# Optimization experiments

Measured on AMD Instinct MI355X. Metric: run time of the kernel, lower is better.

The kernel has to match this reference:

```python
import jax, jax.numpy as jnp
import numpy as np


def _gru_layer(x, W_ih, W_hh, b_ih, b_hh):
    # x: [B, T, in]; W_ih: [3H, in]; W_hh: [3H, H]; gate order (r, z, n) as in PyTorch.
    B, T, _ = x.shape
    H = W_hh.shape[1]
    # Precompute input-side gate pre-activations for the whole sequence (batched GEMM).
    gi = jnp.einsum('bti,gi->btg', x, W_ih) + b_ih  # [B, T, 3H]

    def step(h, gi_t):
        gh = h @ W_hh.T + b_hh                      # [B, 3H]
        i_r, i_z, i_n = jnp.split(gi_t, 3, axis=-1)
        h_r, h_z, h_n = jnp.split(gh, 3, axis=-1)
        r = jax.nn.sigmoid(i_r + h_r)
        z = jax.nn.sigmoid(i_z + h_z)
        n = jnp.tanh(i_n + r * h_n)
        h_new = (1.0 - z) * n + z * h
        return h_new, h_new

    h0 = jnp.zeros((B, H), x.dtype)
    _, hs = jax.lax.scan(step, h0, jnp.swapaxes(gi, 0, 1))  # hs: [T, B, H]
    return jnp.swapaxes(hs, 0, 1)                            # [B, T, H]


def setup_inputs() -> dict:
    key = jax.random.key(0)
    ks = jax.random.split(key, 11)
    B, T, I, H, O = 512, 512, 64, 128, 1
    s = 0.1  # keep gate pre-activations out of saturation
    return {
        'x':     jax.random.normal(ks[0], (B, T, I), jnp.float32),
        'W_ih0': jax.random.normal(ks[1], (3 * H, I), jnp.float32) * s,
        'W_hh0': jax.random.normal(ks[2], (3 * H, H), jnp.float32) * s,
        'b_ih0': jax.random.normal(ks[3], (3 * H,), jnp.float32) * s,
        'b_hh0': jax.random.normal(ks[4], (3 * H,), jnp.float32) * s,
        'W_ih1': jax.random.normal(ks[5], (3 * H, H), jnp.float32) * s,
        'W_hh1': jax.random.normal(ks[6], (3 * H, H), jnp.float32) * s,
        'b_ih1': jax.random.normal(ks[7], (3 * H,), jnp.float32) * s,
        'b_hh1': jax.random.normal(ks[8], (3 * H,), jnp.float32) * s,
        'W_fc':  jax.random.normal(ks[9], (O, H), jnp.float32) * s,
        'b_fc':  jax.random.normal(ks[10], (O,), jnp.float32) * s,
    }


def reference(x, W_ih0, W_hh0, b_ih0, b_hh0, W_ih1, W_hh1, b_ih1, b_hh1, W_fc, b_fc):
    h1 = _gru_layer(x, W_ih0, W_hh0, b_ih0, b_hh0)   # [B, T, H]
    h2 = _gru_layer(h1, W_ih1, W_hh1, b_ih1, b_hh1)  # [B, T, H]
    return h2[:, -1, :] @ W_fc.T + b_fc               # [B, O]
```

## Files before the change

kernel.cpp:

```cpp
#include <hip/hip_runtime.h>
#include <stdint.h>

typedef __bf16 bf16x8 __attribute__((ext_vector_type(8)));
typedef float  floatx4 __attribute__((ext_vector_type(4)));
typedef int    i32x4  __attribute__((ext_vector_type(4)));

#define T_LEN 512
#define NG    (T_LEN / 4)
#define BT    4
#define NTHR  1024
#define XS    72
#define HIS   144
#define HFS   132

#if __has_builtin(__builtin_amdgcn_exp2f)
#define EXP2(x) __builtin_amdgcn_exp2f(x)
#else
#define EXP2(x) exp2f(x)
#endif

#define MFMA_BF(a,b,c)  __builtin_amdgcn_mfma_f32_16x16x32_bf16((a),(b),(c),0,0,0)
#define MFMA_I8(a,b,c)  __builtin_amdgcn_mfma_i32_16x16x64_i8((a),(b),(c),0,0,0)

#define BARRIER_LDS() asm volatile("s_waitcnt lgkmcnt(0)\n\ts_barrier" ::: "memory")

#define L2E   1.4426950408889634f
#define S_RZ  (-L2E / (254.f * 127.f))
#define S_N   (-2.f * L2E / (254.f * 127.f))

__device__ __forceinline__ float rcpf(float x) { return __builtin_amdgcn_rcpf(x); }

__device__ __forceinline__ bf16x8 wfrag_bf(const float* W, int ldk, int row, int k0, float scale) {
    const float* p = W + (size_t)row * ldk + k0;
    bf16x8 r;
    #pragma unroll
    for (int j = 0; j < 8; ++j) r[j] = (__bf16)(p[j] * scale);
    return r;
}
__device__ __forceinline__ i32x4 wfrag_i8(const float* W, int ldk, int row, int k0) {
    const float* p = W + (size_t)row * ldk + k0;
    i32x4 r;
    #pragma unroll
    for (int d = 0; d < 4; ++d) {
        uint32_t dw = 0;
        #pragma unroll
        for (int j = 0; j < 4; ++j) {
            float q = __builtin_rintf(p[d * 4 + j] * 254.f);
            q = fminf(127.f, fmaxf(-127.f, q));
            dw |= ((uint32_t)((int)q & 0xff)) << (8 * j);
        }
        r[d] = (int)dw;
    }
    return r;
}

__global__ __launch_bounds__(NTHR, 4) void gru_fused(
    const float* __restrict__ x,
    const float* __restrict__ Wih0, const float* __restrict__ Whh0,
    const float* __restrict__ bih0, const float* __restrict__ bhh0,
    const float* __restrict__ Wih1, const float* __restrict__ Whh1,
    const float* __restrict__ bih1, const float* __restrict__ bhh1,
    const float* __restrict__ Wfc,  const float* __restrict__ bfc,
    float* __restrict__ out)
{
    __shared__ __align__(16) __bf16      xg[2][16 * XS];
    __shared__ __align__(16) signed char h0b[2][16 * HIS];
    __shared__ __align__(16) signed char h0g[2][16 * HIS];
    __shared__ __align__(16) signed char h1b[2][16 * HIS];
    __shared__ __align__(16) float       hfin[16 * HFS];

    const int tid  = threadIdx.x;
    const int lane = tid & 63;
    const int ln16 = lane & 15;
    const int quad = lane >> 4;
    const int q8   = quad * 8;
    const int q16  = quad * 16;
    const int wave = tid >> 6;
    const int brow = blockIdx.x * BT;

    for (int i = tid; i < 16 * HIS; i += NTHR) {
        h0b[0][i] = 0; h0b[1][i] = 0;
        h0g[0][i] = 0; h0g[1][i] = 0;
        h1b[0][i] = 0; h1b[1][i] = 0;
    }
    for (int i = tid; i < 16 * XS; i += NTHR) {
        xg[0][i] = (__bf16)0.f; xg[1][i] = (__bf16)0.f;
    }
    __syncthreads();

    if (wave < 8) {
        const int c = wave * 16 + ln16;
        const float bNi = -2.f * L2E * bih0[256 + c];
        const float bNh = -2.f * L2E * bhh0[256 + c];
        const float bR  = -L2E * (bih0[c] + bhh0[c]);
        const float bZ  = -L2E * (bih0[128 + c] + bhh0[128 + c]);
        bf16x8 wI[3][2];
        i32x4  wH[3][2];
        #pragma unroll
        for (int g = 0; g < 3; ++g) {
            const int row = g * 128 + c;
            const float sc = (g == 2) ? (-2.f * L2E) : (-L2E);
            #pragma unroll
            for (int q = 0; q < 2; ++q) {
                wI[g][q] = wfrag_bf(Wih0, 64, row, q * 32 + q8, sc);
                wH[g][q] = wfrag_i8(Whh0, 128, row, q * 64 + q16);
            }
        }

        const bool loader = (lane < 32);
        const int lidx = wave * 32 + lane;
        const int sb = (lidx >> 6) & 3, scg = lidx & 63;
        const float* xp = x + (size_t)(brow + sb) * T_LEN * 64 + scg;
        float vx0 = 0.f, vx1 = 0.f, vx2 = 0.f;
        if (loader) {
            #pragma unroll
            for (int tq = 0; tq < 4; ++tq)
                xg[0][(tq + 4 * sb) * XS + scg] = (__bf16)xp[(size_t)tq * 64];
            vx0 = xp[4 * 64];
            vx1 = xp[5 * 64];
            vx2 = xp[6 * 64];
        }
        __syncthreads();

        float hfv = 0.f;
        floatx4 pR, pZ, pNi;
        for (int G = 0; G <= NG; ++G) {
            const bool act = (G < NG);
            #pragma unroll
            for (int p = 0; p < 4; ++p) {
                const int tt = 4 * G + p;
                __builtin_amdgcn_sched_barrier(0);
                BARRIER_LDS();
                if (loader) {
                    if (tt + 4 < T_LEN)
                        xg[(G + 1) & 1][(p + 4 * sb) * XS + scg] = (__bf16)vx0;
                    vx0 = vx1; vx1 = vx2;
                    int tl = tt + 7; if (tl > T_LEN - 1) tl = T_LEN - 1;
                    vx2 = xp[(size_t)tl * 64];
                }
                if (act) {
                    if (p == 0) {
                        bf16x8 ax0 = *(const bf16x8*)&xg[G & 1][ln16 * XS + q8];
                        bf16x8 ax1 = *(const bf16x8*)&xg[G & 1][ln16 * XS + 32 + q8];
                        floatx4 fR  = {bR, bR, bR, bR};
                        floatx4 fZ  = {bZ, bZ, bZ, bZ};
                        floatx4 fNi = {bNi, bNi, bNi, bNi};
                        fR  = MFMA_BF(ax0, wI[0][0], fR);  fR  = MFMA_BF(ax1, wI[0][1], fR);
                        fZ  = MFMA_BF(ax0, wI[1][0], fZ);  fZ  = MFMA_BF(ax1, wI[1][1], fZ);
                        fNi = MFMA_BF(ax0, wI[2][0], fNi); fNi = MFMA_BF(ax1, wI[2][1], fNi);
                        pR = fR; pZ = fZ; pNi = fNi;
                    }
                    const int Rp = (tt + 1) & 1, Wc = tt & 1;
                    i32x4 ah[2];
                    #pragma unroll
                    for (int q = 0; q < 2; ++q)
                        ah[q] = *(const i32x4*)&h0b[Rp][ln16 * HIS + q * 64 + q16];
                    i32x4 cR = {0,0,0,0}, cZ = {0,0,0,0}, cNh = {0,0,0,0};
                    #pragma unroll
                    for (int q = 0; q < 2; ++q) {
                        cR  = MFMA_I8(ah[q], wH[0][q], cR);
                        cZ  = MFMA_I8(ah[q], wH[1][q], cZ);
                        cNh = MFMA_I8(ah[q], wH[2][q], cNh);
                    }
                    const float pr  = fmaf((float)cR[0],  S_RZ, pR[p]);
                    const float pz  = fmaf((float)cZ[0],  S_RZ, pZ[p]);
                    const float phn = fmaf((float)cNh[0], S_N,  bNh);
                    const float r = rcpf(1.f + EXP2(pr));
                    const float z = rcpf(1.f + EXP2(pz));
                    const float n = 2.f * rcpf(1.f + EXP2(fmaf(r, phn, pNi[p]))) - 1.f;
                    const float h = n + z * (hfv - n);
                    hfv = h;
                    const signed char qv = (signed char)(int)__builtin_rintf(h * 127.f);
                    h0b[Wc][(quad * 4) * HIS + c] = qv;
                    h0g[G & 1][(p + 4 * quad) * HIS + c] = qv;
                }
            }
        }
    } else {
        const int wv = wave - 8;
        const int c  = wv * 16 + ln16;
        const float bNi1 = -2.f * L2E * bih1[256 + c];
        const float bNh1 = -2.f * L2E * bhh1[256 + c];
        const float bR1  = -L2E * (bih1[c] + bhh1[c]);
        const float bZ1  = -L2E * (bih1[128 + c] + bhh1[128 + c]);
        i32x4 wI[3][2], wH[3][2];
        #pragma unroll
        for (int g = 0; g < 3; ++g) {
            const int row = g * 128 + c;
            #pragma unroll
            for (int q = 0; q < 2; ++q) {
                wI[g][q] = wfrag_i8(Wih1, 128, row, q * 64 + q16);
                wH[g][q] = wfrag_i8(Whh1, 128, row, q * 64 + q16);
            }
        }
        __syncthreads();

        float hfv = 0.f;
        i32x4 gR, gZ, gNi;
        for (int G = 0; G <= NG; ++G) {
            const bool act = (G >= 1);
            #pragma unroll
            for (int p = 0; p < 4; ++p) {
                __builtin_amdgcn_sched_barrier(0);
                BARRIER_LDS();
                if (act) {
                    if (p == 0) {
                        i32x4 ag[2];
                        #pragma unroll
                        for (int q = 0; q < 2; ++q)
                            ag[q] = *(const i32x4*)&h0g[(G - 1) & 1][ln16 * HIS + q * 64 + q16];
                        i32x4 aR = {0,0,0,0}, aZ = {0,0,0,0}, aN = {0,0,0,0};
                        #pragma unroll
                        for (int q = 0; q < 2; ++q) {
                            aR = MFMA_I8(ag[q], wI[0][q], aR);
                            aZ = MFMA_I8(ag[q], wI[1][q], aZ);
                            aN = MFMA_I8(ag[q], wI[2][q], aN);
                        }
                        gR = aR; gZ = aZ; gNi = aN;
                    }
                    const int s  = 4 * (G - 1) + p;
                    const int Rp = (s + 1) & 1, Wc = s & 1;
                    i32x4 a1[2];
                    #pragma unroll
                    for (int q = 0; q < 2; ++q)
                        a1[q] = *(const i32x4*)&h1b[Rp][ln16 * HIS + q * 64 + q16];
                    i32x4 cR = {0,0,0,0}, cZ = {0,0,0,0}, cNh = {0,0,0,0};
                    #pragma unroll
                    for (int q = 0; q < 2; ++q) {
                        cR  = MFMA_I8(a1[q], wH[0][q], cR);
                        cZ  = MFMA_I8(a1[q], wH[1][q], cZ);
                        cNh = MFMA_I8(a1[q], wH[2][q], cNh);
                    }
                    const float pr  = fmaf((float)(cR[0] + gR[p]), S_RZ, bR1);
                    const float pz  = fmaf((float)(cZ[0] + gZ[p]), S_RZ, bZ1);
                    const float pin = fmaf((float)gNi[p], S_N, bNi1);
                    const float phn = fmaf((float)cNh[0], S_N, bNh1);
                    const float r = rcpf(1.f + EXP2(pr));
                    const float z = rcpf(1.f + EXP2(pz));
                    const float n = 2.f * rcpf(1.f + EXP2(fmaf(r, phn, pin))) - 1.f;
                    const float h = n + z * (hfv - n);
                    hfv = h;
                    h1b[Wc][(quad * 4) * HIS + c] =
                        (signed char)(int)__builtin_rintf(h * 127.f);
                }
            }
        }
        hfin[(quad * 4) * HFS + c] = hfv;
    }

    __syncthreads();
    {
        const int row = tid >> 5, l = tid & 31;
        if (row < 16 && (row & 3) == 0) {
            float s = 0.f;
            #pragma unroll
            for (int k = 0; k < 4; ++k)
                s += hfin[row * HFS + l + 32 * k] * Wfc[l + 32 * k];
            #pragma unroll
            for (int d = 16; d >= 1; d >>= 1) s += __shfl_down(s, d, 32);
            if (l == 0) out[brow + (row >> 2)] = s + bfc[0];
        }
    }
}

extern "C" void kernel_launch(void* const* d_in, const int* in_sizes, int n_in,
                              void* d_out, int out_size, void* d_ws, size_t ws_size,
                              hipStream_t stream) {
    const float* x    = (const float*)d_in[0];
    const float* Wih0 = (const float*)d_in[1];
    const float* Whh0 = (const float*)d_in[2];
    const float* bih0 = (const float*)d_in[3];
    const float* bhh0 = (const float*)d_in[4];
    const float* Wih1 = (const float*)d_in[5];
    const float* Whh1 = (const float*)d_in[6];
    const float* bih1 = (const float*)d_in[7];
    const float* bhh1 = (const float*)d_in[8];
    const float* Wfc  = (const float*)d_in[9];
    const float* bfc  = (const float*)d_in[10];
    float* out = (float*)d_out;

    hipLaunchKernelGGL(gru_fused, dim3(512 / BT), dim3(NTHR), 0, stream,
                       x, Wih0, Whh0, bih0, bhh0, Wih1, Whh1, bih1, bhh1, Wfc, bfc, out);
}
```

Before: 351.3 us.

## Software-pipeline input-projection MFMAs one group ahead, spread across steps

The input-side gate projections for the next 4-step group are now computed one group early, split so that each of steps p=1..3 handles one gate, instead of running all six MFMAs at step p=0 on the critical path. Layer 1 is delayed by one extra group (s = tt-8) so its input projection from h0g is likewise precomputed. The x loader work moves to all 16 waves using 16 lanes each, and x is prefetched two groups ahead. s_setprio is raised around the MFMA section. This adds registers and an extra loop iteration, but evens out per-step latency in the serial recurrence.

```diff
diff --git a/kernel.cpp b/kernel.cpp
--- a/kernel.cpp
+++ b/kernel.cpp
@@ -88,6 +88,20 @@
     }
     __syncthreads();
 
+    const bool loader = (lane < 16);
+    const int lidx = wave * 16 + ln16;
+    const int sb = (lidx >> 6) & 3, scg = lidx & 63;
+    const float* xp = x + (size_t)(brow + sb) * T_LEN * 64 + scg;
+    float vx0 = 0.f, vx1 = 0.f, vx2 = 0.f;
+    if (loader) {
+        #pragma unroll
+        for (int t = 0; t < 8; ++t)
+            xg[t >> 2][((t & 3) + 4 * sb) * XS + scg] = (__bf16)xp[(size_t)t * 64];
+        vx0 = xp[8 * 64];
+        vx1 = xp[9 * 64];
+        vx2 = xp[10 * 64];
+    }
+
     if (wave < 8) {
         const int c = wave * 16 + ln16;
         const float bNi = -2.f * L2E * bih0[256 + c];
@@ -106,55 +120,66 @@
                 wH[g][q] = wfrag_i8(Whh0, 128, row, q * 64 + q16);
             }
         }
-
-        const bool loader = (lane < 32);
-        const int lidx = wave * 32 + lane;
-        const int sb = (lidx >> 6) & 3, scg = lidx & 63;
-        const float* xp = x + (size_t)(brow + sb) * T_LEN * 64 + scg;
-        float vx0 = 0.f, vx1 = 0.f, vx2 = 0.f;
-        if (loader) {
-            #pragma unroll
-            for (int tq = 0; tq < 4; ++tq)
-                xg[0][(tq + 4 * sb) * XS + scg] = (__bf16)xp[(size_t)tq * 64];
-            vx0 = xp[4 * 64];
-            vx1 = xp[5 * 64];
-            vx2 = xp[6 * 64];
-        }
         __syncthreads();
 
         float hfv = 0.f;
-        floatx4 pR, pZ, pNi;
-        for (int G = 0; G <= NG; ++G) {
-            const bool act = (G < NG);
+        floatx4 pcR, pcZ, pcN;
+        floatx4 pnR, pnZ, pnN;
+        bf16x8 gx0, gx1;
+        {
+            bf16x8 ax0 = *(const bf16x8*)&xg[0][ln16 * XS + q8];
+            bf16x8 ax1 = *(const bf16x8*)&xg[0][ln16 * XS + 32 + q8];
+            floatx4 fR  = {bR, bR, bR, bR};
+            floatx4 fZ  = {bZ, bZ, bZ, bZ};
+            floatx4 fN  = {bNi, bNi, bNi, bNi};
+            fR = MFMA_BF(ax0, wI[0][0], fR); fR = MFMA_BF(ax1, wI[0][1], fR);
+            fZ = MFMA_BF(ax0, wI[1][0], fZ); fZ = MFMA_BF(ax1, wI[1][1], fZ);
+            fN = MFMA_BF(ax0, wI[2][0], fN); fN = MFMA_BF(ax1, wI[2][1], fN);
+            pcR = fR; pcZ = fZ; pcN = fN;
+        }
+
+        for (int G = 0; G <= NG + 1; ++G) {
             #pragma unroll
             for (int p = 0; p < 4; ++p) {
                 const int tt = 4 * G + p;
                 __builtin_amdgcn_sched_barrier(0);
                 BARRIER_LDS();
                 if (loader) {
-                    if (tt + 4 < T_LEN)
-                        xg[(G + 1) & 1][(p + 4 * sb) * XS + scg] = (__bf16)vx0;
+                    if (tt + 8 < T_LEN)
+                        xg[G & 1][(p + 4 * sb) * XS + scg] = (__bf16)vx0;
                     vx0 = vx1; vx1 = vx2;
-                    int tl = tt + 7; if (tl > T_LEN - 1) tl = T_LEN - 1;
+                    int tl = tt + 11; if (tl > T_LEN - 1) tl = T_LEN - 1;
                     vx2 = xp[(size_t)tl * 64];
                 }
-                if (act) {
-                    if (p == 0) {
-                        bf16x8 ax0 = *(const bf16x8*)&xg[G & 1][ln16 * XS + q8];
-                        bf16x8 ax1 = *(const bf16x8*)&xg[G & 1][ln16 * XS + 32 + q8];
-                        floatx4 fR  = {bR, bR, bR, bR};
-                        floatx4 fZ  = {bZ, bZ, bZ, bZ};
-                        floatx4 fNi = {bNi, bNi, bNi, bNi};
-                        fR  = MFMA_BF(ax0, wI[0][0], fR);  fR  = MFMA_BF(ax1, wI[0][1], fR);
-                        fZ  = MFMA_BF(ax0, wI[1][0], fZ);  fZ  = MFMA_BF(ax1, wI[1][1], fZ);
-                        fNi = MFMA_BF(ax0, wI[2][0], fNi); fNi = MFMA_BF(ax1, wI[2][1], fNi);
-                        pR = fR; pZ = fZ; pNi = fNi;
-                    }
+
+                if (G < NG) {
                     const int Rp = (tt + 1) & 1, Wc = tt & 1;
                     i32x4 ah[2];
                     #pragma unroll
                     for (int q = 0; q < 2; ++q)
                         ah[q] = *(const i32x4*)&h0b[Rp][ln16 * HIS + q * 64 + q16];
+                    if (p == 0 && G < NG - 1) {
+                        gx0 = *(const bf16x8*)&xg[(G + 1) & 1][ln16 * XS + q8];
+                        gx1 = *(const bf16x8*)&xg[(G + 1) & 1][ln16 * XS + 32 + q8];
+                    }
+                    __builtin_amdgcn_s_setprio(1);
+                    if (G < NG - 1) {
+                        if (p == 1) {
+                            floatx4 f = {bR, bR, bR, bR};
+                            f = MFMA_BF(gx0, wI[0][0], f); f = MFMA_BF(gx1, wI[0][1], f);
+                            pnR = f;
+                        }
+                        if (p == 2) {
+                            floatx4 f = {bZ, bZ, bZ, bZ};
+                            f = MFMA_BF(gx0, wI[1][0], f); f = MFMA_BF(gx1, wI[1][1], f);
+                            pnZ = f;
+                        }
+                        if (p == 3) {
+                            floatx4 f = {bNi, bNi, bNi, bNi};
+                            f = MFMA_BF(gx0, wI[2][0], f); f = MFMA_BF(gx1, wI[2][1], f);
+                            pnN = f;
+                        }
+                    }
                     i32x4 cR = {0,0,0,0}, cZ = {0,0,0,0}, cNh = {0,0,0,0};
                     #pragma unroll
                     for (int q = 0; q < 2; ++q) {
@@ -162,17 +187,21 @@
                         cZ  = MFMA_I8(ah[q], wH[1][q], cZ);
                         cNh = MFMA_I8(ah[q], wH[2][q], cNh);
                     }
-                    const float pr  = fmaf((float)cR[0],  S_RZ, pR[p]);
-                    const float pz  = fmaf((float)cZ[0],  S_RZ, pZ[p]);
+                    __builtin_amdgcn_s_setprio(0);
+                    const float pr  = fmaf((float)cR[0],  S_RZ, pcR[p]);
+                    const float pz  = fmaf((float)cZ[0],  S_RZ, pcZ[p]);
                     const float phn = fmaf((float)cNh[0], S_N,  bNh);
                     const float r = rcpf(1.f + EXP2(pr));
                     const float z = rcpf(1.f + EXP2(pz));
-                    const float n = 2.f * rcpf(1.f + EXP2(fmaf(r, phn, pNi[p]))) - 1.f;
+                    const float n = 2.f * rcpf(1.f + EXP2(fmaf(r, phn, pcN[p]))) - 1.f;
                     const float h = n + z * (hfv - n);
                     hfv = h;
                     const signed char qv = (signed char)(int)__builtin_rintf(h * 127.f);
                     h0b[Wc][(quad * 4) * HIS + c] = qv;
                     h0g[G & 1][(p + 4 * quad) * HIS + c] = qv;
+                    if (p == 3 && G < NG - 1) {
+                        pcR = pnR; pcZ = pnZ; pcN = pnN;
+                    }
                 }
             }
         }
@@ -196,34 +225,55 @@
         __syncthreads();
 
         float hfv = 0.f;
-        i32x4 gR, gZ, gNi;
-        for (int G = 0; G <= NG; ++G) {
-            const bool act = (G >= 1);
+        i32x4 qcR = {0,0,0,0}, qcZ = {0,0,0,0}, qcN = {0,0,0,0};
+        i32x4 qnR, qnZ, qnN;
+        i32x4 ga[2];
+        for (int G = 0; G <= NG + 1; ++G) {
             #pragma unroll
             for (int p = 0; p < 4; ++p) {
+                const int tt = 4 * G + p;
                 __builtin_amdgcn_sched_barrier(0);
                 BARRIER_LDS();
-                if (act) {
-                    if (p == 0) {
-                        i32x4 ag[2];
-                        #pragma unroll
-                        for (int q = 0; q < 2; ++q)
-                            ag[q] = *(const i32x4*)&h0g[(G - 1) & 1][ln16 * HIS + q * 64 + q16];
-                        i32x4 aR = {0,0,0,0}, aZ = {0,0,0,0}, aN = {0,0,0,0};
-                        #pragma unroll
-                        for (int q = 0; q < 2; ++q) {
-                            aR = MFMA_I8(ag[q], wI[0][q], aR);
-                            aZ = MFMA_I8(ag[q], wI[1][q], aZ);
-                            aN = MFMA_I8(ag[q], wI[2][q], aN);
-                        }
-                        gR = aR; gZ = aZ; gNi = aN;
-                    }
-                    const int s  = 4 * (G - 1) + p;
-                    const int Rp = (s + 1) & 1, Wc = s & 1;
-                    i32x4 a1[2];
+                if (loader) {
+                    if (tt + 8 < T_LEN)
+                        xg[G & 1][(p + 4 * sb) * XS + scg] = (__bf16)vx0;
+                    vx0 = vx1; vx1 = vx2;
+                    int tl = tt + 11; if (tl > T_LEN - 1) tl = T_LEN - 1;
+                    vx2 = xp[(size_t)tl * 64];
+                }
+
+                const int s = tt - 8;
+                const bool grp = (G >= 1 && G <= NG);
+                if (p == 0 && grp) {
+                    ga[0] = *(const i32x4*)&h0g[(G - 1) & 1][ln16 * HIS + q16];
+                    ga[1] = *(const i32x4*)&h0g[(G - 1) & 1][ln16 * HIS + 64 + q16];
+                }
+                i32x4 a1[2];
+                if (s >= 0) {
+                    const int Rp = (s + 1) & 1;
                     #pragma unroll
                     for (int q = 0; q < 2; ++q)
                         a1[q] = *(const i32x4*)&h1b[Rp][ln16 * HIS + q * 64 + q16];
+                }
+                __builtin_amdgcn_s_setprio(1);
+                if (grp) {
+                    if (p == 1) {
+                        i32x4 a = {0,0,0,0};
+                        a = MFMA_I8(ga[0], wI[0][0], a); a = MFMA_I8(ga[1], wI[0][1], a);
+                        qnR = a;
+                    }
+                    if (p == 2) {
+                        i32x4 a = {0,0,0,0};
+                        a = MFMA_I8(ga[0], wI[1][0], a); a = MFMA_I8(ga[1], wI[1][1], a);
+                        qnZ = a;
+                    }
+                    if (p == 3) {
+                        i32x4 a = {0,0,0,0};
+                        a = MFMA_I8(ga[0], wI[2][0], a); a = MFMA_I8(ga[1], wI[2][1], a);
+                        qnN = a;
+                    }
+                }
+                if (s >= 0) {
                     i32x4 cR = {0,0,0,0}, cZ = {0,0,0,0}, cNh = {0,0,0,0};
                     #pragma unroll
                     for (int q = 0; q < 2; ++q) {
@@ -231,17 +281,23 @@
                         cZ  = MFMA_I8(a1[q], wH[1][q], cZ);
                         cNh = MFMA_I8(a1[q], wH[2][q], cNh);
                     }
-                    const float pr  = fmaf((float)(cR[0] + gR[p]), S_RZ, bR1);
-                    const float pz  = fmaf((float)(cZ[0] + gZ[p]), S_RZ, bZ1);
-                    const float pin = fmaf((float)gNi[p], S_N, bNi1);
+                    __builtin_amdgcn_s_setprio(0);
+                    const float pr  = fmaf((float)(cR[0] + qcR[p]), S_RZ, bR1);
+                    const float pz  = fmaf((float)(cZ[0] + qcZ[p]), S_RZ, bZ1);
+                    const float pin = fmaf((float)qcN[p], S_N, bNi1);
                     const float phn = fmaf((float)cNh[0], S_N, bNh1);
                     const float r = rcpf(1.f + EXP2(pr));
                     const float z = rcpf(1.f + EXP2(pz));
                     const float n = 2.f * rcpf(1.f + EXP2(fmaf(r, phn, pin))) - 1.f;
                     const float h = n + z * (hfv - n);
                     hfv = h;
-                    h1b[Wc][(quad * 4) * HIS + c] =
+                    h1b[s & 1][(quad * 4) * HIS + c] =
                         (signed char)(int)__builtin_rintf(h * 127.f);
+                } else {
+                    __builtin_amdgcn_s_setprio(0);
+                }
+                if (p == 3 && grp) {
+                    qcR = qnR; qcZ = qnZ; qcN = qnN;
                 }
             }
         }
```

New measurement: 660.0 us. 1.88x slower.

## Skew GRU input-projection groups off the recurrent critical path and spread x loading

Applied to the files above, without the earlier changes.

Both layer wave-groups now compute the grouped input-side MFMA projection one phase ahead of when it is consumed (layer 0 at p==0 for the next group, layer 1 at p==2 with a 7-step lag), holding the results in carried registers. This keeps the input GEMM from sitting directly in front of the dependent recurrent step within the same barrier interval. The x prefetch is also moved out of the layer-0 branch so all 16 waves load 16 lanes each instead of 8 waves loading 32 lanes, and one initial __syncthreads is removed. In exchange the loop runs extra iterations to drain the skew, and the index arithmetic becomes more fragile.

```diff
diff --git a/kernel.cpp b/kernel.cpp
--- a/kernel.cpp
+++ b/kernel.cpp
@@ -7,6 +7,7 @@
 
 #define T_LEN 512
 #define NG    (T_LEN / 4)
+#define NGK   (NG + 1)
 #define BT    4
 #define NTHR  1024
 #define XS    72
@@ -88,6 +89,20 @@
     }
     __syncthreads();
 
+    const bool loader = (lane < 16);
+    const int lidx = wave * 16 + ln16;
+    const int sb = (lidx >> 6) & 3, scg = lidx & 63;
+    const float* xp = x + (size_t)(brow + sb) * T_LEN * 64 + scg;
+    float vx0 = 0.f, vx1 = 0.f, vx2 = 0.f;
+    if (loader) {
+        #pragma unroll
+        for (int t = 0; t < 4; ++t)
+            xg[0][(t + 4 * sb) * XS + scg] = (__bf16)xp[(size_t)t * 64];
+        vx0 = xp[4 * 64];
+        vx1 = xp[5 * 64];
+        vx2 = xp[6 * 64];
+    }
+
     if (wave < 8) {
         const int c = wave * 16 + ln16;
         const float bNi = -2.f * L2E * bih0[256 + c];
@@ -107,54 +122,43 @@
             }
         }
 
-        const bool loader = (lane < 32);
-        const int lidx = wave * 32 + lane;
-        const int sb = (lidx >> 6) & 3, scg = lidx & 63;
-        const float* xp = x + (size_t)(brow + sb) * T_LEN * 64 + scg;
-        float vx0 = 0.f, vx1 = 0.f, vx2 = 0.f;
-        if (loader) {
-            #pragma unroll
-            for (int tq = 0; tq < 4; ++tq)
-                xg[0][(tq + 4 * sb) * XS + scg] = (__bf16)xp[(size_t)tq * 64];
-            vx0 = xp[4 * 64];
-            vx1 = xp[5 * 64];
-            vx2 = xp[6 * 64];
-        }
-        __syncthreads();
-
         float hfv = 0.f;
-        floatx4 pR, pZ, pNi;
-        for (int G = 0; G <= NG; ++G) {
-            const bool act = (G < NG);
+        floatx4 pcR = {0.f,0.f,0.f,0.f}, pcZ = {0.f,0.f,0.f,0.f}, pcN = {0.f,0.f,0.f,0.f};
+
+        for (int G = 0; G <= NGK; ++G) {
             #pragma unroll
             for (int p = 0; p < 4; ++p) {
-                const int tt = 4 * G + p;
+                const int k = 4 * G + p;
                 __builtin_amdgcn_sched_barrier(0);
                 BARRIER_LDS();
                 if (loader) {
-                    if (tt + 4 < T_LEN)
+                    if (k + 4 < T_LEN)
                         xg[(G + 1) & 1][(p + 4 * sb) * XS + scg] = (__bf16)vx0;
                     vx0 = vx1; vx1 = vx2;
-                    int tl = tt + 7; if (tl > T_LEN - 1) tl = T_LEN - 1;
+                    int tl = k + 7; if (tl > T_LEN - 1) tl = T_LEN - 1;
                     vx2 = xp[(size_t)tl * 64];
                 }
-                if (act) {
-                    if (p == 0) {
-                        bf16x8 ax0 = *(const bf16x8*)&xg[G & 1][ln16 * XS + q8];
-                        bf16x8 ax1 = *(const bf16x8*)&xg[G & 1][ln16 * XS + 32 + q8];
-                        floatx4 fR  = {bR, bR, bR, bR};
-                        floatx4 fZ  = {bZ, bZ, bZ, bZ};
-                        floatx4 fNi = {bNi, bNi, bNi, bNi};
-                        fR  = MFMA_BF(ax0, wI[0][0], fR);  fR  = MFMA_BF(ax1, wI[0][1], fR);
-                        fZ  = MFMA_BF(ax0, wI[1][0], fZ);  fZ  = MFMA_BF(ax1, wI[1][1], fZ);
-                        fNi = MFMA_BF(ax0, wI[2][0], fNi); fNi = MFMA_BF(ax1, wI[2][1], fNi);
-                        pR = fR; pZ = fZ; pNi = fNi;
-                    }
-                    const int Rp = (tt + 1) & 1, Wc = tt & 1;
+
+                floatx4 pnR, pnZ, pnN;
+                const bool doGrp = (p == 0) && (G < NG);
+                if (doGrp) {
+                    bf16x8 gx0 = *(const bf16x8*)&xg[G & 1][ln16 * XS + q8];
+                    bf16x8 gx1 = *(const bf16x8*)&xg[G & 1][ln16 * XS + 32 + q8];
+                    floatx4 fR  = {bR, bR, bR, bR};
+                    floatx4 fZ  = {bZ, bZ, bZ, bZ};
+                    floatx4 fN  = {bNi, bNi, bNi, bNi};
+                    fR = MFMA_BF(gx0, wI[0][0], fR); fR = MFMA_BF(gx1, wI[0][1], fR);
+                    fZ = MFMA_BF(gx0, wI[1][0], fZ); fZ = MFMA_BF(gx1, wI[1][1], fZ);
+                    fN = MFMA_BF(gx0, wI[2][0], fN); fN = MFMA_BF(gx1, wI[2][1], fN);
+                    pnR = fR; pnZ = fZ; pnN = fN;
+                }
+
+                const int t = k - 1;
+                if (t >= 0 && t < T_LEN) {
                     i32x4 ah[2];
                     #pragma unroll
                     for (int q = 0; q < 2; ++q)
-                        ah[q] = *(const i32x4*)&h0b[Rp][ln16 * HIS + q * 64 + q16];
+                        ah[q] = *(const i32x4*)&h0b[p & 1][ln16 * HIS + q * 64 + q16];
                     i32x4 cR = {0,0,0,0}, cZ = {0,0,0,0}, cNh = {0,0,0,0};
                     #pragma unroll
                     for (int q = 0; q < 2; ++q) {
@@ -162,17 +166,20 @@
                         cZ  = MFMA_I8(ah[q], wH[1][q], cZ);
                         cNh = MFMA_I8(ah[q], wH[2][q], cNh);
                     }
-                    const float pr  = fmaf((float)cR[0],  S_RZ, pR[p]);
-                    const float pz  = fmaf((float)cZ[0],  S_RZ, pZ[p]);
+                    const float pr  = fmaf((float)cR[0],  S_RZ, pcR[(p + 3) & 3]);
+                    const float pz  = fmaf((float)cZ[0],  S_RZ, pcZ[(p + 3) & 3]);
                     const float phn = fmaf((float)cNh[0], S_N,  bNh);
                     const float r = rcpf(1.f + EXP2(pr));
                     const float z = rcpf(1.f + EXP2(pz));
-                    const float n = 2.f * rcpf(1.f + EXP2(fmaf(r, phn, pNi[p]))) - 1.f;
+                    const float n = 2.f * rcpf(1.f + EXP2(fmaf(r, phn, pcN[(p + 3) & 3]))) - 1.f;
                     const float h = n + z * (hfv - n);
                     hfv = h;
                     const signed char qv = (signed char)(int)__builtin_rintf(h * 127.f);
-                    h0b[Wc][(quad * 4) * HIS + c] = qv;
-                    h0g[G & 1][(p + 4 * quad) * HIS + c] = qv;
+                    h0b[(p + 1) & 1][(quad * 4) * HIS + c] = qv;
+                    h0g[((unsigned)t >> 2) & 1][(((p + 3) & 3) + 4 * quad) * HIS + c] = qv;
+                }
+                if (doGrp) {
+                    pcR = pnR; pcZ = pnZ; pcN = pnN;
                 }
             }
         }
@@ -193,37 +200,43 @@
                 wH[g][q] = wfrag_i8(Whh1, 128, row, q * 64 + q16);
             }
         }
-        __syncthreads();
 
         float hfv = 0.f;
-        i32x4 gR, gZ, gNi;
-        for (int G = 0; G <= NG; ++G) {
-            const bool act = (G >= 1);
+        i32x4 qcR = {0,0,0,0}, qcZ = {0,0,0,0}, qcN = {0,0,0,0};
+
+        for (int G = 0; G <= NGK; ++G) {
             #pragma unroll
             for (int p = 0; p < 4; ++p) {
+                const int k = 4 * G + p;
                 __builtin_amdgcn_sched_barrier(0);
                 BARRIER_LDS();
-                if (act) {
-                    if (p == 0) {
-                        i32x4 ag[2];
-                        #pragma unroll
-                        for (int q = 0; q < 2; ++q)
-                            ag[q] = *(const i32x4*)&h0g[(G - 1) & 1][ln16 * HIS + q * 64 + q16];
-                        i32x4 aR = {0,0,0,0}, aZ = {0,0,0,0}, aN = {0,0,0,0};
-                        #pragma unroll
-                        for (int q = 0; q < 2; ++q) {
-                            aR = MFMA_I8(ag[q], wI[0][q], aR);
-                            aZ = MFMA_I8(ag[q], wI[1][q], aZ);
-                            aN = MFMA_I8(ag[q], wI[2][q], aN);
-                        }
-                        gR = aR; gZ = aZ; gNi = aN;
-                    }
-                    const int s  = 4 * (G - 1) + p;
-                    const int Rp = (s + 1) & 1, Wc = s & 1;
+                if (loader) {
+                    if (k + 4 < T_LEN)
+                        xg[(G + 1) & 1][(p + 4 * sb) * XS + scg] = (__bf16)vx0;
+                    vx0 = vx1; vx1 = vx2;
+                    int tl = k + 7; if (tl > T_LEN - 1) tl = T_LEN - 1;
+                    vx2 = xp[(size_t)tl * 64];
+                }
+
+                i32x4 qnR, qnZ, qnN;
+                const bool doGrp = (p == 2) && (G >= 1) && (G <= NG);
+                if (doGrp) {
+                    const int g = G - 1;
+                    i32x4 ga0 = *(const i32x4*)&h0g[g & 1][ln16 * HIS + q16];
+                    i32x4 ga1 = *(const i32x4*)&h0g[g & 1][ln16 * HIS + 64 + q16];
+                    i32x4 aR = {0,0,0,0}, aZ = {0,0,0,0}, aN = {0,0,0,0};
+                    aR = MFMA_I8(ga0, wI[0][0], aR); aR = MFMA_I8(ga1, wI[0][1], aR);
+                    aZ = MFMA_I8(ga0, wI[1][0], aZ); aZ = MFMA_I8(ga1, wI[1][1], aZ);
+                    aN = MFMA_I8(ga0, wI[2][0], aN); aN = MFMA_I8(ga1, wI[2][1], aN);
+                    qnR = aR; qnZ = aZ; qnN = aN;
+                }
+
+                const int s = k - 7;
+                if (s >= 0 && s < T_LEN) {
                     i32x4 a1[2];
                     #pragma unroll
                     for (int q = 0; q < 2; ++q)
-                        a1[q] = *(const i32x4*)&h1b[Rp][ln16 * HIS + q * 64 + q16];
+                        a1[q] = *(const i32x4*)&h1b[p & 1][ln16 * HIS + q * 64 + q16];
                     i32x4 cR = {0,0,0,0}, cZ = {0,0,0,0}, cNh = {0,0,0,0};
                     #pragma unroll
                     for (int q = 0; q < 2; ++q) {
@@ -231,17 +244,20 @@
                         cZ  = MFMA_I8(a1[q], wH[1][q], cZ);
                         cNh = MFMA_I8(a1[q], wH[2][q], cNh);
                     }
-                    const float pr  = fmaf((float)(cR[0] + gR[p]), S_RZ, bR1);
-                    const float pz  = fmaf((float)(cZ[0] + gZ[p]), S_RZ, bZ1);
-                    const float pin = fmaf((float)gNi[p], S_N, bNi1);
+                    const float pr  = fmaf((float)(cR[0] + qcR[(p + 1) & 3]), S_RZ, bR1);
+                    const float pz  = fmaf((float)(cZ[0] + qcZ[(p + 1) & 3]), S_RZ, bZ1);
+                    const float pin = fmaf((float)qcN[(p + 1) & 3], S_N, bNi1);
                     const float phn = fmaf((float)cNh[0], S_N, bNh1);
                     const float r = rcpf(1.f + EXP2(pr));
                     const float z = rcpf(1.f + EXP2(pz));
                     const float n = 2.f * rcpf(1.f + EXP2(fmaf(r, phn, pin))) - 1.f;
                     const float h = n + z * (hfv - n);
                     hfv = h;
-                    h1b[Wc][(quad * 4) * HIS + c] =
+                    h1b[(p + 1) & 1][(quad * 4) * HIS + c] =
                         (signed char)(int)__builtin_rintf(h * 127.f);
+                }
+                if (doGrp) {
+                    qcR = qnR; qcZ = qnZ; qcN = qnN;
                 }
             }
         }
```

New measurement: 562.8 us. +60.2%, slower.
